# Performance work log

Hardware: AMD Instinct MI355X
Metric: run time of the kernel (lower is better)

## Reference

```python
import jax, jax.numpy as jnp
import numpy as np
import math

N = 65536   # number of tree nodes
K = 4       # branching factor of the complete K-ary tree
D = 300     # input_size
H = 256     # hidden_size

def _levels(n, k):
    # complete k-ary tree: level l spans [start, start + k**l)
    levels, start, size = [], 0, 1
    while start < n:
        end = min(start + size, n)
        levels.append((start, end))
        start, size = end, size * k
    return levels

LEVELS = _levels(N, K)

def setup_inputs() -> dict:
    key = jax.random.key(0)
    ks = jax.random.split(key, 16)
    def U(k, shape, s):
        return jax.random.uniform(k, shape, jnp.float32, -s, s)
    s1 = 1.0 / math.sqrt(D + H)
    sfi = 1.0 / math.sqrt(D)
    sfh = 1.0 / math.sqrt(H)
    return {
        "inputs": jax.random.normal(ks[0], (N, D), jnp.float32),
        "ix_w": U(ks[1], (H, D), s1), "ix_b": U(ks[2], (H,), s1),
        "ih_w": U(ks[3], (H, H), s1), "ih_b": U(ks[4], (H,), s1),
        "ux_w": U(ks[5], (H, D), s1), "ux_b": U(ks[6], (H,), s1),
        "uh_w": U(ks[7], (H, H), s1), "uh_b": U(ks[8], (H,), s1),
        "fi_w": U(ks[9], (H, D), sfi), "fi_b": U(ks[10], (H,), sfi),
        "fh_w": U(ks[11], (H, H), sfh), "fh_b": U(ks[12], (H,), sfh),
    }

def reference(inputs, ix_w, ix_b, ih_w, ih_b, ux_w, ux_b, uh_w, uh_b,
              fi_w, fi_b, fh_w, fh_b):
    # Precompute all input projections once (batched over every node).
    ix = inputs @ ix_w.T + ix_b   # [N, H]
    ux = inputs @ ux_w.T + ux_b   # [N, H]
    fi = inputs @ fi_w.T + fi_b   # [N, H]
    h = jnp.zeros((N, H), inputs.dtype)
    c = jnp.zeros((N, H), inputs.dtype)
    # Bottom-up over tree levels (children before parents); level bounds static.
    for (s, e) in reversed(LEVELS):
        node = jnp.arange(s, e)                                   # [L]
        cidx = node[:, None] * K + 1 + jnp.arange(K)[None, :]     # [L, K]
        valid = cidx < N
        cidx = jnp.where(valid, cidx, 0)
        m = valid[..., None].astype(inputs.dtype)                 # [L, K, 1]
        hc = h[cidx] * m                                          # [L, K, H]
        cc = c[cidx] * m
        h_sum = hc.sum(axis=1)                                    # [L, H]
        # per-child forget gate: sigmoid(W_fi x + b_fi + W_fh h_k + b_fh)
        f = jax.nn.sigmoid(fi[s:e][:, None, :]
                           + jnp.einsum('lkh,gh->lkg', hc, fh_w) + fh_b)
        fc = (f * cc).sum(axis=1)                                 # masked via cc
        i = jax.nn.sigmoid(ix[s:e] + h_sum @ ih_w.T + ih_b)
        u = jnp.tanh(ux[s:e] + h_sum @ uh_w.T + uh_b)
        c_new = i * u + fc
        h_new = jnp.tanh(c_new)          # no output gate in this module
        h = h.at[s:e].set(h_new)
        c = c.at[s:e].set(c_new)
    # root node state (matches (next_h, [next_h, next_c]) at the root)
    return h[0], c[0]
```

## Files before the change

### kernel.cpp

```cpp
#include <hip/hip_runtime.h>
#include <hip/hip_bf16.h>


#define NTOT 65536
#define DD   300
#define KP   320
#define HH   256
#define LEAF_START 16384
#define LOG2E 1.4426950408889634f

typedef unsigned short u16;
typedef unsigned int   u32;
typedef __attribute__((ext_vector_type(8))) short bf16x8;
typedef __attribute__((ext_vector_type(4))) float f32x4;

union BF8 { bf16x8 v; u16 u[8]; };

#define OFF_HB    0ull
#define OFF_CB    33554944ull
#define OFF_PRE   67109888ull
#define OFF_WXB   92275712ull
#define OFF_WHB   92767232ull
#define OFF_XB    93160448ull
#define OFF_PIU   135103488ull
#define OFF_FC    146375680ull
#define OFF_HSB   157647872ull
#define OFF_BI    166102016ull
#define OFF_BU    166103040ull
#define OFF_BF    166104064ull

__device__ __forceinline__ float frcp(float x) { return __builtin_amdgcn_rcpf(x); }
__device__ __forceinline__ float fex2(float x) { return __builtin_amdgcn_exp2f(x); }
__device__ __forceinline__ float sigm(float x)  { return frcp(1.f + fex2(-LOG2E * x)); }
__device__ __forceinline__ float ftanh(float x) { return 1.f - 2.f * frcp(1.f + fex2(2.f * LOG2E * x)); }

__device__ __forceinline__ u16 f2bf(float f) {
    __hip_bfloat16 b = __float2bfloat16(f);
    u16 u; __builtin_memcpy(&u, &b, 2); return u;
}
__device__ __forceinline__ float bf2f(u16 b) {
    union { u32 u; float f; } v; v.u = ((u32)b) << 16;
    return v.f;
}
__device__ __forceinline__ int lidx(int r, int g) { return (r << 3) | (g ^ (r & 7)); }

__device__ __forceinline__ void gll16(const void* g, void* l) {
    __builtin_amdgcn_global_load_lds(
        (const __attribute__((address_space(1))) unsigned int*)g,
        (__attribute__((address_space(3))) unsigned int*)l, 16, 0, 0);
}

__global__ __launch_bounds__(256) void conv_all(
    const float* __restrict__ X,
    const float* __restrict__ ixw, const float* __restrict__ uxw,
    const float* __restrict__ fiw,
    const float* __restrict__ ihw, const float* __restrict__ uhw,
    const float* __restrict__ fhw,
    const float* __restrict__ ixb, const float* __restrict__ ihb,
    const float* __restrict__ uxb, const float* __restrict__ uhb,
    const float* __restrict__ fib, const float* __restrict__ fhb,
    u32* __restrict__ Xb2, u32* __restrict__ Wxb2, u32* __restrict__ Whb2,
    u16* __restrict__ hb, u16* __restrict__ cb,
    float* __restrict__ bI, float* __restrict__ bU, float* __restrict__ bF)
{
    const int b = blockIdx.x;
    const int t = threadIdx.x;
    if (b < 2048) {
        const size_t total = (size_t)NTOT * 160;
        for (size_t id = (size_t)b * 256 + t; id < total; id += (size_t)2048 * 256) {
            const int node = (int)(id / 160);
            const int k    = ((int)(id % 160)) * 2;
            const float f0 = (k < DD)     ? X[(size_t)node * DD + k]     : 0.f;
            const float f1 = (k + 1 < DD) ? X[(size_t)node * DD + k + 1] : 0.f;
            Xb2[id] = (u32)f2bf(f0) | ((u32)f2bf(f1) << 16);
        }
    } else if (b < 2528) {
        const int b2 = b - 2048;
        const int total = 768 * 160;
        for (int id = b2 * 256 + t; id < total; id += 480 * 256) {
            const int row = id / 160;
            const int k   = (id % 160) * 2;
            const float* src = (row < 256) ? (ixw + (size_t)row * DD)
                             : (row < 512) ? (uxw + (size_t)(row - 256) * DD)
                                           : (fiw + (size_t)(row - 512) * DD);
            const float f0 = (k < DD)     ? src[k]     : 0.f;
            const float f1 = (k + 1 < DD) ? src[k + 1] : 0.f;
            Wxb2[id] = (u32)f2bf(f0) | ((u32)f2bf(f1) << 16);
        }
    } else {
        const int b3 = b - 2528;
        if (b3 == 0) {
            hb[(size_t)NTOT * HH + t] = 0;
            cb[(size_t)NTOT * HH + t] = 0;
            bI[t] = ixb[t] + ihb[t];
            bU[t] = uxb[t] + uhb[t];
            bF[t] = fib[t] + fhb[t];
        }
        const int total = 768 * 128;
        for (int id = b3 * 256 + t; id < total; id += 384 * 256) {
            const int row = id / 128;
            const int k   = (id % 128) * 2;
            const float* src = (row < 256) ? (ihw + (size_t)row * HH)
                             : (row < 512) ? (uhw + (size_t)(row - 256) * HH)
                                           : (fhw + (size_t)(row - 512) * HH);
            Whb2[id] = (u32)f2bf(src[k]) | ((u32)f2bf(src[k + 1]) << 16);
        }
    }
}

__global__ __launch_bounds__(256) void lp_gemm(
    const u16* __restrict__ Xb, const u16* __restrict__ Wxb,
    const float* __restrict__ bI, const float* __restrict__ bU,
    u16* __restrict__ hb, u16* __restrict__ cb, u16* __restrict__ pre)
{
    __shared__ bf16x8 Ash[2048];
    __shared__ bf16x8 Bsh[2048];

    const int tid  = threadIdx.x;
    const int lane = tid & 63;
    const int w    = tid >> 6;
    const int wr   = w >> 1, wc = w & 1;
    const int m16  = lane & 15, q = lane >> 4;

    const bf16x8* __restrict__ Xv = (const bf16x8*)Xb;
    const bf16x8* __restrict__ Wv = (const bf16x8*)Wxb;

    if (blockIdx.x < 1536) {
        const int xcd = blockIdx.x & 7, tt = blockIdx.x >> 3;
        const int c = tt & 3, rg = tt >> 2;
        const int row0   = LEAF_START + (rg * 8 + xcd) * 128;
        const int chbase = c * 64;

        auto stage = [&](int kt, int buf) {
            const int base = buf << 10;
            #pragma unroll
            for (int i = 0; i < 4; ++i) {
                const int sI = w * 256 + i * 64 + lane;
                const int r = sI >> 3, gs = sI & 7;
                const int g = gs ^ (r & 7);
                gll16(Xv + (size_t)(row0 + r) * 40 + kt * 8 + g, &Ash[base + sI]);
            }
            #pragma unroll
            for (int i = 0; i < 4; ++i) {
                const int sI = w * 256 + i * 64 + lane;
                const int br = sI >> 3, gs = sI & 7;
                const int g = gs ^ (br & 7);
                const int srow = ((br >> 6) << 8) + chbase + (br & 63);
                gll16(Wv + (size_t)srow * 40 + kt * 8 + g, &Bsh[base + sI]);
            }
        };

        f32x4 accI[4][2], accU[4][2];
        #pragma unroll
        for (int mf = 0; mf < 4; ++mf)
            #pragma unroll
            for (int nf = 0; nf < 2; ++nf) { accI[mf][nf] = (f32x4)0.f; accU[mf][nf] = (f32x4)0.f; }

        stage(0, 0);
        __syncthreads();
        for (int kt = 0; kt < 5; ++kt) {
            const int cur = kt & 1;
            if (kt < 4) stage(kt + 1, cur ^ 1);
            const int base = cur << 10;
            #pragma unroll
            for (int ks = 0; ks < 2; ++ks) {
                const int kg = ks * 4 + q;
                bf16x8 a[4], bIv[2], bUv[2];
                #pragma unroll
                for (int mf = 0; mf < 4; ++mf)
                    a[mf] = Ash[base + lidx(wr * 64 + mf * 16 + m16, kg)];
                #pragma unroll
                for (int nf = 0; nf < 2; ++nf) {
                    bIv[nf] = Bsh[base + lidx(wc * 32 + nf * 16 + m16, kg)];
                    bUv[nf] = Bsh[base + lidx(64 + wc * 32 + nf * 16 + m16, kg)];
                }
                #pragma unroll
                for (int mf = 0; mf < 4; ++mf)
                    #pragma unroll
                    for (int nf = 0; nf < 2; ++nf) {
                        accI[mf][nf] = __builtin_amdgcn_mfma_f32_16x16x32_bf16(
                            a[mf], bIv[nf], accI[mf][nf], 0, 0, 0);
                        accU[mf][nf] = __builtin_amdgcn_mfma_f32_16x16x32_bf16(
                            a[mf], bUv[nf], accU[mf][nf], 0, 0, 0);
                    }
            }
            __syncthreads();
        }

        #pragma unroll
        for (int nf = 0; nf < 2; ++nf) {
            const int ch = chbase + wc * 32 + nf * 16 + m16;
            const float bi = bI[ch];
            const float bu = bU[ch];
            #pragma unroll
            for (int mf = 0; mf < 4; ++mf) {
                #pragma unroll
                for (int r4 = 0; r4 < 4; ++r4) {
                    const float cn = sigm(accI[mf][nf][r4] + bi) * ftanh(accU[mf][nf][r4] + bu);
                    const int node = row0 + wr * 64 + mf * 16 + q * 4 + r4;
                    const size_t off = (size_t)node * HH + ch;
                    cb[off] = f2bf(cn);
                    hb[off] = f2bf(ftanh(cn));
                }
            }
        }
    } else {
        const int B2 = blockIdx.x - 1536;
        const int xcd = B2 & 7, tt = B2 >> 3;
        const int c = tt % 6, rg = tt / 6;
        const int row0 = (rg * 8 + xcd) * 128;
        const int n0   = c * 128;

        auto stage = [&](int kt, int buf) {
            const int base = buf << 10;
            #pragma unroll
            for (int i = 0; i < 4; ++i) {
                const int sI = w * 256 + i * 64 + lane;
                const int r = sI >> 3, gs = sI & 7;
                const int g = gs ^ (r & 7);
                gll16(Xv + (size_t)(row0 + r) * 40 + kt * 8 + g, &Ash[base + sI]);
            }
            #pragma unroll
            for (int i = 0; i < 4; ++i) {
                const int sI = w * 256 + i * 64 + lane;
                const int br = sI >> 3, gs = sI & 7;
                const int g = gs ^ (br & 7);
                gll16(Wv + (size_t)(n0 + br) * 40 + kt * 8 + g, &Bsh[base + sI]);
            }
        };

        f32x4 acc[4][4];
        #pragma unroll
        for (int mf = 0; mf < 4; ++mf)
            #pragma unroll
            for (int nf = 0; nf < 4; ++nf) acc[mf][nf] = (f32x4)0.f;

        stage(0, 0);
        __syncthreads();
        for (int kt = 0; kt < 5; ++kt) {
            const int cur = kt & 1;
            if (kt < 4) stage(kt + 1, cur ^ 1);
            const int base = cur << 10;
            #pragma unroll
            for (int ks = 0; ks < 2; ++ks) {
                const int kg = ks * 4 + q;
                bf16x8 a[4], b[4];
                #pragma unroll
                for (int mf = 0; mf < 4; ++mf)
                    a[mf] = Ash[base + lidx(wr * 64 + mf * 16 + m16, kg)];
                #pragma unroll
                for (int nf = 0; nf < 4; ++nf)
                    b[nf] = Bsh[base + lidx(wc * 64 + nf * 16 + m16, kg)];
                #pragma unroll
                for (int mf = 0; mf < 4; ++mf)
                    #pragma unroll
                    for (int nf = 0; nf < 4; ++nf)
                        acc[mf][nf] = __builtin_amdgcn_mfma_f32_16x16x32_bf16(
                            a[mf], b[nf], acc[mf][nf], 0, 0, 0);
            }
            __syncthreads();
        }

        #pragma unroll
        for (int mf = 0; mf < 4; ++mf)
            #pragma unroll
            for (int nf = 0; nf < 4; ++nf) {
                const int col = n0 + wc * 64 + nf * 16 + m16;
                #pragma unroll
                for (int r4 = 0; r4 < 4; ++r4) {
                    const int node = row0 + wr * 64 + mf * 16 + q * 4 + r4;
                    pre[(size_t)node * 768 + col] = f2bf(acc[mf][nf][r4]);
                }
            }
    }
}

__global__ __launch_bounds__(256) void rec_gemm(
    const u16* __restrict__ hb, const u16* __restrict__ hsb,
    const u16* __restrict__ Whb, const u16* __restrict__ pre,
    const float* __restrict__ bF, const u16* __restrict__ cb,
    u16* __restrict__ projIU, float* __restrict__ fcbuf,
    int s, int crow0, int L, int bigIU)
{
    __shared__ bf16x8 Ash[2048];
    __shared__ bf16x8 Bsh[2048];

    const int nIUrb = (L + 127) >> 7;
    const int bid   = blockIdx.x;

    bool isIU; int rb, cbk;
    if (bid < nIUrb * 4) { isIU = true;  rb = bid >> 2; cbk = bid & 3; }
    else { isIU = false; const int b2 = bid - nIUrb * 4; rb = b2 >> 1; cbk = b2 & 1; }

    const int row0  = rb * 128;
    const int Brow0 = isIU ? cbk * 128 : 512 + cbk * 128;
    const int ocol0 = cbk * 128;

    const int tid  = threadIdx.x;
    const int lane = tid & 63;
    const int w    = tid >> 6;
    const int wr   = w >> 1, wc = w & 1;
    const int m16  = lane & 15, q = lane >> 4;

    const bf16x8* __restrict__ Hv = (const bf16x8*)hb;
    const bf16x8* __restrict__ Sv = (const bf16x8*)hsb;
    const bf16x8* __restrict__ Wv = (const bf16x8*)Whb;

    auto stage = [&](int kt, int buf) {
        const int base = buf << 10;
        if (isIU && bigIU) {
            #pragma unroll
            for (int i = 0; i < 4; ++i) {
                const int G = tid + i * 256;
                const int r = G >> 3, g = G & 7;
                bf16x8 val;
                if (row0 + r < L) {
                    const size_t cg0 = (size_t)(crow0 + 4 * (row0 + r)) * 32 + kt * 8 + g;
                    BF8 x0, x1, x2, x3, o;
                    x0.v = Hv[cg0]; x1.v = Hv[cg0 + 32];
                    x2.v = Hv[cg0 + 64]; x3.v = Hv[cg0 + 96];
                    #pragma unroll
                    for (int j = 0; j < 8; ++j)
                        o.u[j] = f2bf(bf2f(x0.u[j]) + bf2f(x1.u[j])
                                    + bf2f(x2.u[j]) + bf2f(x3.u[j]));
                    val = o.v;
                } else {
                    BF8 z;
                    #pragma unroll
                    for (int j = 0; j < 8; ++j) z.u[j] = 0;
                    val = z.v;
                }
                Ash[base + lidx(r, g)] = val;
            }
        } else {
            #pragma unroll
            for (int i = 0; i < 4; ++i) {
                const int sI = w * 256 + i * 64 + lane;
                const int r = sI >> 3, gs = sI & 7;
                const int g = gs ^ (r & 7);
                if (isIU) {
                    gll16(Sv + (size_t)(s + row0 + r) * 32 + kt * 8 + g, &Ash[base + sI]);
                } else {
                    int arow = crow0 + row0 + r;
                    if (arow > NTOT) arow = NTOT;
                    gll16(Hv + (size_t)arow * 32 + kt * 8 + g, &Ash[base + sI]);
                }
            }
        }
        #pragma unroll
        for (int i = 0; i < 4; ++i) {
            const int sI = w * 256 + i * 64 + lane;
            const int br = sI >> 3, gs = sI & 7;
            const int g = gs ^ (br & 7);
            gll16(Wv + (size_t)(Brow0 + br) * 32 + kt * 8 + g, &Bsh[base + sI]);
        }
    };

    f32x4 acc[4][4];
    #pragma unroll
    for (int mf = 0; mf < 4; ++mf)
        #pragma unroll
        for (int nf = 0; nf < 4; ++nf) acc[mf][nf] = (f32x4)0.f;

    stage(0, 0);
    __syncthreads();
    for (int kt = 0; kt < 4; ++kt) {
        const int cur = kt & 1;
        if (kt < 3) stage(kt + 1, cur ^ 1);
        const int base = cur << 10;
        #pragma unroll
        for (int ks = 0; ks < 2; ++ks) {
            const int kg = ks * 4 + q;
            bf16x8 a[4], b[4];
            #pragma unroll
            for (int mf = 0; mf < 4; ++mf)
                a[mf] = Ash[base + lidx(wr * 64 + mf * 16 + m16, kg)];
            #pragma unroll
            for (int nf = 0; nf < 4; ++nf)
                b[nf] = Bsh[base + lidx(wc * 64 + nf * 16 + m16, kg)];
            #pragma unroll
            for (int mf = 0; mf < 4; ++mf)
                #pragma unroll
                for (int nf = 0; nf < 4; ++nf)
                    acc[mf][nf] = __builtin_amdgcn_mfma_f32_16x16x32_bf16(
                        a[mf], b[nf], acc[mf][nf], 0, 0, 0);
        }
        __syncthreads();
    }

    if (isIU) {
        #pragma unroll
        for (int mf = 0; mf < 4; ++mf)
            #pragma unroll
            for (int nf = 0; nf < 4; ++nf) {
                const int col = ocol0 + wc * 64 + nf * 16 + m16;
                #pragma unroll
                for (int r4 = 0; r4 < 4; ++r4) {
                    const int orow = row0 + wr * 64 + mf * 16 + q * 4 + r4;
                    projIU[(size_t)orow * 512 + col] = f2bf(acc[mf][nf][r4]);
                }
            }
    } else {
        #pragma unroll
        for (int mf = 0; mf < 4; ++mf) {
            const int off  = wr * 64 + mf * 16 + q * 4;
            const int goff = (row0 + off) >> 2;
            if (goff < L) {
                #pragma unroll
                for (int nf = 0; nf < 4; ++nf) {
                    const int col = ocol0 + wc * 64 + nf * 16 + m16;
                    const float fpre = bf2f(pre[(size_t)(s + goff) * 768 + 512 + col]) + bF[col];
                    float fc = 0.f;
                    #pragma unroll
                    for (int r4 = 0; r4 < 4; ++r4) {
                        int child = crow0 + row0 + off + r4;
                        if (child > NTOT) child = NTOT;
                        const float cc = bf2f(cb[(size_t)child * HH + col]);
                        fc = fmaf(sigm(acc[mf][nf][r4] + fpre), cc, fc);
                    }
                    fcbuf[(size_t)goff * HH + col] = fc;
                }
            }
        }
    }
}

__global__ __launch_bounds__(256) void gate_kernel(
    const u32* __restrict__ pre2, const u32* __restrict__ pIU2,
    const float* __restrict__ fcbuf,
    const float* __restrict__ bI, const float* __restrict__ bU,
    u32* __restrict__ hb2, u32* __restrict__ cb2, u32* __restrict__ hsumb2,
    float* __restrict__ out, int s, int L)
{
    const int t  = threadIdx.x;
    const int j2 = t & 127;

    if (L == 1) {
        if (t >= 128) return;
        const float2 vbi = ((const float2*)bI)[j2];
        const float2 vbu = ((const float2*)bU)[j2];
        const u32 pi = pre2[j2];
        const u32 pu = pre2[128 + j2];
        const u32 ri = pIU2[j2];
        const u32 ru = pIU2[128 + j2];
        const float aI0 = bf2f((u16)pi) + bf2f((u16)ri) + vbi.x;
        const float aI1 = bf2f((u16)(pi >> 16)) + bf2f((u16)(ri >> 16)) + vbi.y;
        const float aU0 = bf2f((u16)pu) + bf2f((u16)ru) + vbu.x;
        const float aU1 = bf2f((u16)(pu >> 16)) + bf2f((u16)(ru >> 16)) + vbu.y;
        const float2 fc = ((const float2*)fcbuf)[j2];
        const float cn0 = fmaf(sigm(aI0), ftanh(aU0), fc.x);
        const float cn1 = fmaf(sigm(aI1), ftanh(aU1), fc.y);
        const float hn0 = ftanh(cn0);
        const float hn1 = ftanh(cn1);
        hb2[j2] = (u32)f2bf(hn0) | ((u32)f2bf(hn1) << 16);
        cb2[j2] = (u32)f2bf(cn0) | ((u32)f2bf(cn1) << 16);
        ((float2*)out)[j2] = make_float2(hn0, hn1);
        ((float2*)(out + 256))[j2] = make_float2(cn0, cn1);
        return;
    }

    const int ng = (L + 3) >> 2;
    const int gateBlocks = (ng + 1) >> 1;
    if ((int)blockIdx.x >= gateBlocks) {
        const int id = ((int)blockIdx.x - gateBlocks) * 256 + t;
        if (id < 1365 * 128) {
            const int ploc = id >> 7, jj = id & 127;
            const int p = 4096 + ploc;
            const int c0 = 4 * p + 1;
            float s0 = 0.f, s1 = 0.f;
            #pragma unroll
            for (int k = 0; k < 4; ++k) {
                const u32 v = hb2[(size_t)(c0 + k) * 128 + jj];
                s0 += bf2f((u16)v);
                s1 += bf2f((u16)(v >> 16));
            }
            hsumb2[(size_t)p * 128 + jj] = (u32)f2bf(s0) | ((u32)f2bf(s1) << 16);
        }
        return;
    }

    const float2 vbi = ((const float2*)bI)[j2];
    const float2 vbu = ((const float2*)bU)[j2];
    const int g = blockIdx.x * 2 + (t >> 7);
    if (g >= ng) return;
    const int p = ((s - 1) >> 2) + g;

    float hs0 = 0.f, hs1 = 0.f;
    #pragma unroll
    for (int k = 0; k < 4; ++k) {
        const int nloc = 4 * g + k;
        const int n = s + nloc;
        if (nloc < L) {
            const u32 pi = pre2[(size_t)n * 384 + j2];
            const u32 pu = pre2[(size_t)n * 384 + 128 + j2];
            const u32 ri = pIU2[(size_t)nloc * 256 + j2];
            const u32 ru = pIU2[(size_t)nloc * 256 + 128 + j2];
            const float aI0 = bf2f((u16)pi) + bf2f((u16)ri) + vbi.x;
            const float aI1 = bf2f((u16)(pi >> 16)) + bf2f((u16)(ri >> 16)) + vbi.y;
            const float aU0 = bf2f((u16)pu) + bf2f((u16)ru) + vbu.x;
            const float aU1 = bf2f((u16)(pu >> 16)) + bf2f((u16)(ru >> 16)) + vbu.y;
            const float2 fc = ((const float2*)fcbuf)[(size_t)nloc * 128 + j2];
            const float cn0 = fmaf(sigm(aI0), ftanh(aU0), fc.x);
            const float cn1 = fmaf(sigm(aI1), ftanh(aU1), fc.y);
            const float hn0 = ftanh(cn0);
            const float hn1 = ftanh(cn1);
            hb2[(size_t)n * 128 + j2] = (u32)f2bf(hn0) | ((u32)f2bf(hn1) << 16);
            cb2[(size_t)n * 128 + j2] = (u32)f2bf(cn0) | ((u32)f2bf(cn1) << 16);
            hs0 += hn0; hs1 += hn1;
        } else {
            const u32 v = hb2[(size_t)n * 128 + j2];
            hs0 += bf2f((u16)v);
            hs1 += bf2f((u16)(v >> 16));
        }
    }
    hsumb2[(size_t)p * 128 + j2] = (u32)f2bf(hs0) | ((u32)f2bf(hs1) << 16);
}

extern "C" void kernel_launch(void* const* d_in, const int* in_sizes, int n_in,
                              void* d_out, int out_size, void* d_ws, size_t ws_size,
                              hipStream_t stream) {
    const float* X   = (const float*)d_in[0];
    const float* ixw = (const float*)d_in[1];
    const float* ixb = (const float*)d_in[2];
    const float* ihw = (const float*)d_in[3];
    const float* ihb = (const float*)d_in[4];
    const float* uxw = (const float*)d_in[5];
    const float* uxb = (const float*)d_in[6];
    const float* uhw = (const float*)d_in[7];
    const float* uhb = (const float*)d_in[8];
    const float* fiw = (const float*)d_in[9];
    const float* fib = (const float*)d_in[10];
    const float* fhw = (const float*)d_in[11];
    const float* fhb = (const float*)d_in[12];
    float* out = (float*)d_out;

    char* ws = (char*)d_ws;
    u16* hb   = (u16*)(ws + OFF_HB);
    u16* cb   = (u16*)(ws + OFF_CB);
    u16* pre  = (u16*)(ws + OFF_PRE);
    u16* Wxb  = (u16*)(ws + OFF_WXB);
    u16* Whb  = (u16*)(ws + OFF_WHB);
    u16* Xb   = (u16*)(ws + OFF_XB);
    u16* pIU  = (u16*)(ws + OFF_PIU);
    float* fc = (float*)(ws + OFF_FC);
    u16* hsb  = (u16*)(ws + OFF_HSB);
    float* bI = (float*)(ws + OFF_BI);
    float* bU = (float*)(ws + OFF_BU);
    float* bF = (float*)(ws + OFF_BF);

    conv_all<<<2912, 256, 0, stream>>>(X, ixw, uxw, fiw, ihw, uhw, fhw,
        ixb, ihb, uxb, uhb, fib, fhb,
        (u32*)Xb, (u32*)Wxb, (u32*)Whb, hb, cb, bI, bU, bF);

    lp_gemm<<<2304, 256, 0, stream>>>(Xb, Wxb, bI, bU, hb, cb, pre);

    const int starts[8] = {5461, 1365, 341, 85, 21, 5, 1, 0};
    const int ends[8]   = {16384, 5461, 1365, 341, 85, 21, 5, 1};
    for (int l = 0; l < 8; ++l) {
        const int s = starts[l], e = ends[l];
        const int L = e - s;
        const int crow0 = 4 * s + 1;
        const int nIUrb = (L + 127) >> 7;
        const int nFrb  = (4 * L + 127) >> 7;
        rec_gemm<<<nIUrb * 4 + nFrb * 2, 256, 0, stream>>>(hb, hsb, Whb, pre, bF, cb,
            pIU, fc, s, crow0, L, (l == 0) ? 1 : 0);
        const int ng = (L + 3) >> 2;
        const int gateBlocks = (ng + 1) >> 1;
        const int hsBlocks = (l == 0) ? 683 : 0;
        gate_kernel<<<gateBlocks + hsBlocks, 256, 0, stream>>>(
            (const u32*)pre, (const u32*)pIU, fc, bI, bU,
            (u32*)hb, (u32*)cb, (u32*)hsb, out, s, L);
    }
}
```

Baseline: 186.6 us.

## Fuse recurrent GEMM and gate into one kernel per upper tree level

For the seven smaller tree levels, the separate rec_gemm and gate_kernel launches are replaced by a single level_kernel. Each block handles 32 parents: it computes the child forget-gate GEMM and keeps fc in shared memory, then runs the i/u GEMM on the child h-sums and applies the gates, writing h, c and the parent h-sum directly. This halves the launches for those levels and drops the global round-trip through the fc and pIU buffers. The cost is fewer blocks per level and a heavier per-block schedule with many syncthreads.

```diff
diff --git a/kernel.cpp b/kernel.cpp
--- a/kernel.cpp
+++ b/kernel.cpp
@@ -43,6 +43,7 @@
     return v.f;
 }
 __device__ __forceinline__ int lidx(int r, int g) { return (r << 3) | (g ^ (r & 7)); }
+__device__ __forceinline__ int lidx4(int r, int g) { return (r << 2) | (g ^ (r & 3)); }
 
 __device__ __forceinline__ void gll16(const void* g, void* l) {
     __builtin_amdgcn_global_load_lds(
@@ -434,30 +435,6 @@
 {
     const int t  = threadIdx.x;
     const int j2 = t & 127;
-
-    if (L == 1) {
-        if (t >= 128) return;
-        const float2 vbi = ((const float2*)bI)[j2];
-        const float2 vbu = ((const float2*)bU)[j2];
-        const u32 pi = pre2[j2];
-        const u32 pu = pre2[128 + j2];
-        const u32 ri = pIU2[j2];
-        const u32 ru = pIU2[128 + j2];
-        const float aI0 = bf2f((u16)pi) + bf2f((u16)ri) + vbi.x;
-        const float aI1 = bf2f((u16)(pi >> 16)) + bf2f((u16)(ri >> 16)) + vbi.y;
-        const float aU0 = bf2f((u16)pu) + bf2f((u16)ru) + vbu.x;
-        const float aU1 = bf2f((u16)(pu >> 16)) + bf2f((u16)(ru >> 16)) + vbu.y;
-        const float2 fc = ((const float2*)fcbuf)[j2];
-        const float cn0 = fmaf(sigm(aI0), ftanh(aU0), fc.x);
-        const float cn1 = fmaf(sigm(aI1), ftanh(aU1), fc.y);
-        const float hn0 = ftanh(cn0);
-        const float hn1 = ftanh(cn1);
-        hb2[j2] = (u32)f2bf(hn0) | ((u32)f2bf(hn1) << 16);
-        cb2[j2] = (u32)f2bf(cn0) | ((u32)f2bf(cn1) << 16);
-        ((float2*)out)[j2] = make_float2(hn0, hn1);
-        ((float2*)(out + 256))[j2] = make_float2(cn0, cn1);
-        return;
-    }
 
     const int ng = (L + 3) >> 2;
     const int gateBlocks = (ng + 1) >> 1;
@@ -516,6 +493,192 @@
     hsumb2[(size_t)p * 128 + j2] = (u32)f2bf(hs0) | ((u32)f2bf(hs1) << 16);
 }
 
+__global__ __launch_bounds__(256) void level_kernel(
+    u16* __restrict__ hb, u16* __restrict__ cb, u16* __restrict__ hsb,
+    const u16* __restrict__ Whb, const u16* __restrict__ pre,
+    const float* __restrict__ bI, const float* __restrict__ bU,
+    const float* __restrict__ bF,
+    float* __restrict__ out, int s, int crow0, int L)
+{
+    __shared__ float  fcs[32 * 256];
+    __shared__ bf16x8 Abuf[512];
+    __shared__ bf16x8 Bbuf[1024];
+
+    const int tid  = threadIdx.x;
+    const int lane = tid & 63;
+    const int w    = tid >> 6;
+    const int m16  = lane & 15, q = lane >> 4;
+    const int b    = blockIdx.x;
+    const int p0   = 32 * b;
+
+    const bf16x8* __restrict__ Hv = (const bf16x8*)hb;
+    const bf16x8* __restrict__ Sv = (const bf16x8*)hsb;
+    const bf16x8* __restrict__ Wv = (const bf16x8*)Whb;
+
+    f32x4 accF[8][4];
+    #pragma unroll
+    for (int mf = 0; mf < 8; ++mf)
+        #pragma unroll
+        for (int nf = 0; nf < 4; ++nf) accF[mf][nf] = (f32x4)0.f;
+
+    for (int kt = 0; kt < 8; ++kt) {
+        __syncthreads();
+        #pragma unroll
+        for (int i = 0; i < 2; ++i) {
+            const int sI = w * 128 + i * 64 + lane;
+            const int r = sI >> 2, gs = sI & 3;
+            const int g = gs ^ (r & 3);
+            int child = crow0 + 128 * b + r;
+            if (child > NTOT) child = NTOT;
+            gll16(Hv + (size_t)child * 32 + kt * 4 + g, &Abuf[sI]);
+        }
+        #pragma unroll
+        for (int i = 0; i < 4; ++i) {
+            const int sI = w * 256 + i * 64 + lane;
+            const int r = sI >> 2, gs = sI & 3;
+            const int g = gs ^ (r & 3);
+            gll16(Wv + (size_t)(512 + r) * 32 + kt * 4 + g, &Bbuf[sI]);
+        }
+        __syncthreads();
+        bf16x8 a[8], bb[4];
+        #pragma unroll
+        for (int mf = 0; mf < 8; ++mf) {
+            const int R = mf * 16 + m16;
+            a[mf] = Abuf[lidx4(R, q)];
+        }
+        #pragma unroll
+        for (int nf = 0; nf < 4; ++nf) {
+            const int R = 64 * w + nf * 16 + m16;
+            bb[nf] = Bbuf[lidx4(R, q)];
+        }
+        #pragma unroll
+        for (int mf = 0; mf < 8; ++mf)
+            #pragma unroll
+            for (int nf = 0; nf < 4; ++nf)
+                accF[mf][nf] = __builtin_amdgcn_mfma_f32_16x16x32_bf16(
+                    a[mf], bb[nf], accF[mf][nf], 0, 0, 0);
+    }
+    __syncthreads();
+
+    #pragma unroll
+    for (int mf = 0; mf < 8; ++mf) {
+        const int par = mf * 4 + q;
+        if (p0 + par < L) {
+            const int chrow = mf * 16 + q * 4;
+            #pragma unroll
+            for (int nf = 0; nf < 4; ++nf) {
+                const int col = 64 * w + nf * 16 + m16;
+                const float fpre = bf2f(pre[(size_t)(s + p0 + par) * 768 + 512 + col]) + bF[col];
+                float fc = 0.f;
+                #pragma unroll
+                for (int r4 = 0; r4 < 4; ++r4) {
+                    int child = crow0 + 128 * b + chrow + r4;
+                    if (child > NTOT) child = NTOT;
+                    const float cc = bf2f(cb[(size_t)child * HH + col]);
+                    fc = fmaf(sigm(accF[mf][nf][r4] + fpre), cc, fc);
+                }
+                fcs[par * 256 + col] = fc;
+            }
+        }
+    }
+
+    f32x4 accIU[2][8];
+    #pragma unroll
+    for (int mf = 0; mf < 2; ++mf)
+        #pragma unroll
+        for (int nf = 0; nf < 8; ++nf) accIU[mf][nf] = (f32x4)0.f;
+
+    for (int kt = 0; kt < 8; ++kt) {
+        __syncthreads();
+        if (lane < 32) {
+            const int sI = w * 32 + lane;
+            const int r = sI >> 2, gs = sI & 3;
+            const int g = gs ^ (r & 3);
+            gll16(Sv + (size_t)(s + p0 + r) * 32 + kt * 4 + g, &Abuf[sI]);
+        }
+        #pragma unroll
+        for (int i = 0; i < 4; ++i) {
+            const int sI = w * 256 + i * 64 + lane;
+            const int r = sI >> 2, gs = sI & 3;
+            const int g = gs ^ (r & 3);
+            gll16(Wv + (size_t)r * 32 + kt * 4 + g, &Bbuf[sI]);
+        }
+        __syncthreads();
+        bf16x8 a2[2], b2[4];
+        #pragma unroll
+        for (int mf = 0; mf < 2; ++mf) {
+            const int R = mf * 16 + m16;
+            a2[mf] = Abuf[lidx4(R, q)];
+        }
+        #pragma unroll
+        for (int nf = 0; nf < 4; ++nf) {
+            const int R = 64 * w + nf * 16 + m16;
+            b2[nf] = Bbuf[lidx4(R, q)];
+        }
+        #pragma unroll
+        for (int mf = 0; mf < 2; ++mf)
+            #pragma unroll
+            for (int nf = 0; nf < 4; ++nf)
+                accIU[mf][nf] = __builtin_amdgcn_mfma_f32_16x16x32_bf16(
+                    a2[mf], b2[nf], accIU[mf][nf], 0, 0, 0);
+        __syncthreads();
+        #pragma unroll
+        for (int i = 0; i < 4; ++i) {
+            const int sI = w * 256 + i * 64 + lane;
+            const int r = sI >> 2, gs = sI & 3;
+            const int g = gs ^ (r & 3);
+            gll16(Wv + (size_t)(256 + r) * 32 + kt * 4 + g, &Bbuf[sI]);
+        }
+        __syncthreads();
+        #pragma unroll
+        for (int nf = 0; nf < 4; ++nf) {
+            const int R = 64 * w + nf * 16 + m16;
+            b2[nf] = Bbuf[lidx4(R, q)];
+        }
+        #pragma unroll
+        for (int mf = 0; mf < 2; ++mf)
+            #pragma unroll
+            for (int nf = 0; nf < 4; ++nf)
+                accIU[mf][nf + 4] = __builtin_amdgcn_mfma_f32_16x16x32_bf16(
+                    a2[mf], b2[nf], accIU[mf][nf + 4], 0, 0, 0);
+    }
+    __syncthreads();
+
+    #pragma unroll
+    for (int mf2 = 0; mf2 < 2; ++mf2) {
+        #pragma unroll
+        for (int nf = 0; nf < 4; ++nf) {
+            const int c = 64 * w + nf * 16 + m16;
+            float hs = 0.f;
+            #pragma unroll
+            for (int r4 = 0; r4 < 4; ++r4) {
+                const int p = mf2 * 16 + q * 4 + r4;
+                const int n = s + p0 + p;
+                float hn;
+                if (p0 + p < L) {
+                    const float aI = accIU[mf2][nf][r4]
+                                   + bf2f(pre[(size_t)n * 768 + c]) + bI[c];
+                    const float aU = accIU[mf2][nf + 4][r4]
+                                   + bf2f(pre[(size_t)n * 768 + 256 + c]) + bU[c];
+                    const float cn = fmaf(sigm(aI), ftanh(aU), fcs[p * 256 + c]);
+                    hn = ftanh(cn);
+                    hb[(size_t)n * HH + c] = f2bf(hn);
+                    cb[(size_t)n * HH + c] = f2bf(cn);
+                    if (n == 0) { out[c] = hn; out[256 + c] = cn; }
+                } else {
+                    hn = bf2f(hb[(size_t)n * HH + c]);
+                }
+                hs += hn;
+            }
+            const int base = mf2 * 16 + q * 4;
+            if (p0 + base < L) {
+                const int gp = ((s - 1) >> 2) + ((p0 + base) >> 2);
+                hsb[(size_t)gp * HH + c] = f2bf(hs);
+            }
+        }
+    }
+}
+
 extern "C" void kernel_launch(void* const* d_in, const int* in_sizes, int n_in,
                               void* d_out, int out_size, void* d_ws, size_t ws_size,
                               hipStream_t stream) {
@@ -554,21 +717,26 @@
 
     lp_gemm<<<2304, 256, 0, stream>>>(Xb, Wxb, bI, bU, hb, cb, pre);
 
-    const int starts[8] = {5461, 1365, 341, 85, 21, 5, 1, 0};
-    const int ends[8]   = {16384, 5461, 1365, 341, 85, 21, 5, 1};
-    for (int l = 0; l < 8; ++l) {
-        const int s = starts[l], e = ends[l];
-        const int L = e - s;
-        const int crow0 = 4 * s + 1;
+    {
+        const int s = 5461, L = 10923, crow0 = 21845;
         const int nIUrb = (L + 127) >> 7;
         const int nFrb  = (4 * L + 127) >> 7;
         rec_gemm<<<nIUrb * 4 + nFrb * 2, 256, 0, stream>>>(hb, hsb, Whb, pre, bF, cb,
-            pIU, fc, s, crow0, L, (l == 0) ? 1 : 0);
+            pIU, fc, s, crow0, L, 1);
         const int ng = (L + 3) >> 2;
         const int gateBlocks = (ng + 1) >> 1;
-        const int hsBlocks = (l == 0) ? 683 : 0;
-        gate_kernel<<<gateBlocks + hsBlocks, 256, 0, stream>>>(
+        gate_kernel<<<gateBlocks + 683, 256, 0, stream>>>(
             (const u32*)pre, (const u32*)pIU, fc, bI, bU,
             (u32*)hb, (u32*)cb, (u32*)hsb, out, s, L);
     }
-}
+
+    const int starts[7] = {1365, 341, 85, 21, 5, 1, 0};
+    const int Ls[7]     = {4096, 1024, 256, 64, 16, 4, 1};
+    for (int l = 0; l < 7; ++l) {
+        const int s = starts[l], L = Ls[l];
+        const int crow0 = 4 * s + 1;
+        const int nPB = (L + 31) >> 5;
+        level_kernel<<<nPB, 256, 0, stream>>>(hb, cb, hsb, Whb, pre,
+                                              bI, bU, bF, out, s, crow0, L);
+    }
+}
```

After: 289.4 us. 55.1% more time.
